# Performance work log

Measured on AMD Instinct MI355X. Metric: run time of the kernel, lower is better.

## Reference

```python
import jax, jax.numpy as jnp
import numpy as np

NC, M, D = 4, 512, 64
COMMITMENT_COST = 0.25


def setup_inputs() -> dict:
    key = jax.random.key(0)
    k1, k2 = jax.random.split(key)
    N = 65536
    x = jax.random.normal(k1, (N, NC * D), dtype=jnp.float32)
    # original init: uniform(-1/m, 1/m); randn*small keeps comparable scale
    embedding = jax.random.normal(k2, (NC, M, D), dtype=jnp.float32) * (1.0 / M)
    mask = jnp.ones((N, NC), dtype=jnp.float32)
    return {"x": x, "embedding": embedding, "mask": mask}


def reference(x, embedding, mask):
    nc, m, d = embedding.shape
    x_flat = x.reshape(-1, nc, d)                      # (N, nc, d)
    xd = jax.lax.stop_gradient(x_flat)                 # detached copy

    # squared-distance search expressed as a GEMM (same math as sum((x-e)^2)):
    x2 = jnp.sum(xd * xd, axis=-1)[:, :, None]
    e2 = jnp.sum(embedding * embedding, axis=-1)[None, :, :]
    xe = jnp.einsum('ncd,cmd->ncm', xd, embedding)
    distances = x2 - 2.0 * xe + e2

    indices = jnp.argmin(distances, axis=-1)           # (N, nc) int
    # gather nearest code vectors: (N, nc, d)
    quantized = embedding[jnp.arange(nc)[None, :], indices]
    quantized = quantized * mask[..., None]

    codebook_loss = jnp.mean((jax.lax.stop_gradient(x_flat) - quantized) ** 2)
    e_latent_loss = jnp.mean((x_flat - jax.lax.stop_gradient(quantized)) ** 2)
    commitment_loss = COMMITMENT_COST * e_latent_loss

    # straight-through estimator
    quantized_st = x_flat + jax.lax.stop_gradient(quantized - x_flat)
    quantized_st = quantized_st.reshape(x.shape)

    # perplexity via per-codebook histogram (avoids N x nc x m one-hot)
    counts = jax.vmap(lambda idx: jnp.bincount(idx, length=m))(indices.T)  # (nc, m)
    avg_probs = counts.astype(x.dtype) / x_flat.shape[0]
    perplexity = jnp.exp(-jnp.sum(avg_probs * jnp.log(avg_probs + 1e-10)))

    return (quantized_st, commitment_loss, codebook_loss, perplexity, indices)
```

## Files before the change

### kernel.cpp

```cpp
#include <hip/hip_runtime.h>
#include <math.h>
#include <float.h>

#define NTOK 65536
#define NCB  4
#define MCODE 512
#define DIM  64

#define QST_SIZE (NTOK * NCB * DIM)
#define IDX_OFF  (QST_SIZE + 3)

#define TOK_TILE  256
#define XS_STRIDE 68

#define WS_EH 0
#define WS_EL 262144
#define WS_D0 524288
#define WS_CNT 532480
#define WS_LOSS 540672

typedef _Float16 half8 __attribute__((ext_vector_type(8)));
typedef float floatx4 __attribute__((ext_vector_type(4)));

__global__ __launch_bounds__(256) void prep_kernel(const float* __restrict__ emb,
                                                   _Float16* __restrict__ eh,
                                                   _Float16* __restrict__ el,
                                                   float* __restrict__ d0,
                                                   int* __restrict__ counts,
                                                   float* __restrict__ lossSum) {
    int row = blockIdx.x * 256 + threadIdx.x;
    if (row >= NCB * MCODE) return;
    const float* src = emb + (size_t)row * DIM;
    _Float16* ph = eh + (size_t)row * DIM;
    _Float16* pl = el + (size_t)row * DIM;
    float s = 0.f;
#pragma unroll
    for (int j = 0; j < DIM / 8; ++j) {
        half8 h, l;
#pragma unroll
        for (int t = 0; t < 8; ++t) {
            float e = src[j * 8 + t];
            s += e * e;
            float f = e * 512.0f;
            _Float16 hi = (_Float16)f;
            float r = f - (float)hi;
            h[t] = hi;
            l[t] = (_Float16)r;
        }
        *(half8*)(ph + j * 8) = h;
        *(half8*)(pl + j * 8) = l;
    }
    d0[row] = 512.0f * s;
    counts[row] = 0;
    if (row == 0) *lossSum = 0.f;
}

__global__ __launch_bounds__(256) void vq_main(const float* __restrict__ x,
                                               const float* __restrict__ emb,
                                               const float* __restrict__ mask,
                                               const _Float16* __restrict__ eh,
                                               const _Float16* __restrict__ el,
                                               const float* __restrict__ d0,
                                               int* __restrict__ counts,
                                               float* __restrict__ lossSum,
                                               float* __restrict__ outQ,
                                               float* __restrict__ outIdx) {
    __shared__ float Xs[TOK_TILE * XS_STRIDE];
    __shared__ int   Is[TOK_TILE];
    __shared__ float wls[4];

    const int tid  = threadIdx.x;
    const int c    = blockIdx.y;
    const int n0tk = blockIdx.x * TOK_TILE;
    const int lane = tid & 63;
    const int w    = tid >> 6;
    const int col  = lane & 15;
    const int quad = lane >> 4;

#pragma unroll
    for (int i = 0; i < 16; ++i) {
        int q = tid + i * 256;
        int tok = q >> 4, d4 = q & 15;
        float4 v = *(const float4*)(x + (size_t)(n0tk + tok) * (NCB * DIM) + c * DIM + d4 * 4);
        *(float4*)(Xs + tok * XS_STRIDE + d4 * 4) = v;
    }
    __syncthreads();

    half8 Ahi[4][2], Alo[4][2];
#pragma unroll
    for (int s = 0; s < 4; ++s) {
        const float* xr = Xs + (w * 64 + s * 16 + col) * XS_STRIDE;
#pragma unroll
        for (int ks = 0; ks < 2; ++ks) {
            const float* p = xr + ks * 32 + quad * 8;
            half8 h, l;
#pragma unroll
            for (int t = 0; t < 8; ++t) {
                float f = p[t];
                _Float16 hi = (_Float16)f;
                float r = f - (float)hi;
                h[t] = hi;
                l[t] = (_Float16)r;
            }
            Ahi[s][ks] = h;
            Alo[s][ks] = l;
        }
    }

    float minv[4][4];
    int   mini[4][4];
#pragma unroll
    for (int s = 0; s < 4; ++s)
#pragma unroll
        for (int r = 0; r < 4; ++r) { minv[s][r] = FLT_MAX; mini[s][r] = 0; }

    const _Float16* ehc = eh + (size_t)c * MCODE * DIM;
    const _Float16* elc = el + (size_t)c * MCODE * DIM;
    const float*    d0c = d0 + c * MCODE;

#pragma unroll 2
    for (int nt = 0; nt < 32; ++nt) {
        const int nbase = nt * 16;
        const int n = nbase + col;
        const _Float16* bh = ehc + (size_t)n * DIM + quad * 8;
        const _Float16* bl = elc + (size_t)n * DIM + quad * 8;
        half8 Bh0 = *(const half8*)(bh);
        half8 Bh1 = *(const half8*)(bh + 32);
        half8 Bl0 = *(const half8*)(bl);
        half8 Bl1 = *(const half8*)(bl + 32);
        float d0v = d0c[n];

#pragma unroll
        for (int s = 0; s < 4; ++s) {
            floatx4 acc = {0.f, 0.f, 0.f, 0.f};
            acc = __builtin_amdgcn_mfma_f32_16x16x32_f16(Ahi[s][0], Bh0, acc, 0, 0, 0);
            acc = __builtin_amdgcn_mfma_f32_16x16x32_f16(Ahi[s][1], Bh1, acc, 0, 0, 0);
            acc = __builtin_amdgcn_mfma_f32_16x16x32_f16(Alo[s][0], Bh0, acc, 0, 0, 0);
            acc = __builtin_amdgcn_mfma_f32_16x16x32_f16(Alo[s][1], Bh1, acc, 0, 0, 0);
            acc = __builtin_amdgcn_mfma_f32_16x16x32_f16(Ahi[s][0], Bl0, acc, 0, 0, 0);
            acc = __builtin_amdgcn_mfma_f32_16x16x32_f16(Ahi[s][1], Bl1, acc, 0, 0, 0);
#pragma unroll
            for (int r = 0; r < 4; ++r) {
                float dv = fmaf(-2.f, acc[r], d0v);
                if (dv < minv[s][r]) { minv[s][r] = dv; mini[s][r] = n; }
            }
        }
    }

#pragma unroll
    for (int off = 1; off < 16; off <<= 1) {
#pragma unroll
        for (int s = 0; s < 4; ++s)
#pragma unroll
            for (int r = 0; r < 4; ++r) {
                float ov = __shfl_xor(minv[s][r], off);
                int   oi = __shfl_xor(mini[s][r], off);
                if (ov < minv[s][r] || (ov == minv[s][r] && oi < mini[s][r])) {
                    minv[s][r] = ov; mini[s][r] = oi;
                }
            }
    }
    if (col == 0) {
#pragma unroll
        for (int s = 0; s < 4; ++s)
#pragma unroll
            for (int r = 0; r < 4; ++r)
                Is[w * 64 + s * 16 + quad * 4 + r] = mini[s][r];
    }
    __syncthreads();

    {
        int idx = Is[tid];
        atomicAdd(&counts[c * MCODE + idx], 1);
        outIdx[(size_t)(n0tk + tid) * NCB + c] = (float)idx;
    }

    float lloss = 0.f;
#pragma unroll
    for (int i = 0; i < 16; ++i) {
        int q = tid + i * 256;
        int tok = q >> 4, d4 = q & 15;
        int idx = Is[tok];
        float mv = mask[(size_t)(n0tk + tok) * NCB + c];
        float4 e4 = *(const float4*)(emb + ((size_t)c * MCODE + idx) * DIM + d4 * 4);
        float4 x4 = *(const float4*)(Xs + tok * XS_STRIDE + d4 * 4);
        float qx = e4.x * mv, qy = e4.y * mv, qz = e4.z * mv, qw = e4.w * mv;
        float4 o;
        o.x = x4.x + (qx - x4.x);
        o.y = x4.y + (qy - x4.y);
        o.z = x4.z + (qz - x4.z);
        o.w = x4.w + (qw - x4.w);
        *(float4*)(outQ + (size_t)(n0tk + tok) * (NCB * DIM) + c * DIM + d4 * 4) = o;
        float dx = x4.x - qx, dy = x4.y - qy, dz = x4.z - qz, dw = x4.w - qw;
        lloss += dx * dx + dy * dy + dz * dz + dw * dw;
    }
#pragma unroll
    for (int off = 32; off > 0; off >>= 1) lloss += __shfl_xor(lloss, off);
    if ((tid & 63) == 0) wls[tid >> 6] = lloss;
    __syncthreads();
    if (tid == 0) {
        float s = wls[0] + wls[1] + wls[2] + wls[3];
        atomicAdd(lossSum, s);
    }
}

__global__ __launch_bounds__(256) void finalize_kernel(const int* __restrict__ counts,
                                                       const float* __restrict__ lossSum,
                                                       float* __restrict__ out) {
    __shared__ float wls[4];
    int tid = threadIdx.x;
    float s = 0.f;
#pragma unroll
    for (int i = 0; i < 8; ++i) {
        int j = tid + i * 256;
        float p = (float)counts[j] * (1.0f / 65536.0f);
        s += p * logf(p + 1e-10f);
    }
#pragma unroll
    for (int off = 32; off > 0; off >>= 1) s += __shfl_xor(s, off);
    if ((tid & 63) == 0) wls[tid >> 6] = s;
    __syncthreads();
    if (tid == 0) {
        float tot = wls[0] + wls[1] + wls[2] + wls[3];
        float L = *lossSum * (1.0f / (float)QST_SIZE);
        out[QST_SIZE + 0] = 0.25f * L;
        out[QST_SIZE + 1] = L;
        out[QST_SIZE + 2] = expf(-tot);
    }
}

extern "C" void kernel_launch(void* const* d_in, const int* in_sizes, int n_in,
                              void* d_out, int out_size, void* d_ws, size_t ws_size,
                              hipStream_t stream) {
    const float* x    = (const float*)d_in[0];
    const float* emb  = (const float*)d_in[1];
    const float* mask = (const float*)d_in[2];
    float* out = (float*)d_out;

    _Float16* eh   = (_Float16*)((char*)d_ws + WS_EH);
    _Float16* el   = (_Float16*)((char*)d_ws + WS_EL);
    float* d0      = (float*)((char*)d_ws + WS_D0);
    int*   counts  = (int*)((char*)d_ws + WS_CNT);
    float* lossSum = (float*)((char*)d_ws + WS_LOSS);

    prep_kernel<<<dim3(8), dim3(256), 0, stream>>>(emb, eh, el, d0, counts, lossSum);
    vq_main<<<dim3(NTOK / TOK_TILE, NCB), dim3(256), 0, stream>>>(
        x, emb, mask, eh, el, d0, counts, lossSum, out, out + IDX_OFF);
    finalize_kernel<<<dim3(1), dim3(256), 0, stream>>>(counts, lossSum, out);
}
```

Before: 222.3 us.

## Drop LDS staging of x and software-prefetch next codebook tile

Removes the 68KB shared-memory tile for x: the A fragments are now read straight from global memory with float4 loads, and x is re-read from global memory in the epilogue. This frees LDS, which should allow more blocks per CU, and removes one barrier. The codebook loop now double-buffers the B fragments and d0 in registers, loading tile nt+1 while the MFMAs run on tile nt. The cost is extra register pressure and a second global read of x, which will likely hit L2.

```diff
diff --git a/kernel.cpp b/kernel.cpp
--- a/kernel.cpp
+++ b/kernel.cpp
@@ -11,7 +11,6 @@
 #define IDX_OFF  (QST_SIZE + 3)
 
 #define TOK_TILE  256
-#define XS_STRIDE 68
 
 #define WS_EH 0
 #define WS_EL 262144
@@ -65,7 +64,6 @@
                                                float* __restrict__ lossSum,
                                                float* __restrict__ outQ,
                                                float* __restrict__ outIdx) {
-    __shared__ float Xs[TOK_TILE * XS_STRIDE];
     __shared__ int   Is[TOK_TILE];
     __shared__ float wls[4];
 
@@ -77,28 +75,21 @@
     const int col  = lane & 15;
     const int quad = lane >> 4;
 
-#pragma unroll
-    for (int i = 0; i < 16; ++i) {
-        int q = tid + i * 256;
-        int tok = q >> 4, d4 = q & 15;
-        float4 v = *(const float4*)(x + (size_t)(n0tk + tok) * (NCB * DIM) + c * DIM + d4 * 4);
-        *(float4*)(Xs + tok * XS_STRIDE + d4 * 4) = v;
-    }
-    __syncthreads();
-
     half8 Ahi[4][2], Alo[4][2];
 #pragma unroll
     for (int s = 0; s < 4; ++s) {
-        const float* xr = Xs + (w * 64 + s * 16 + col) * XS_STRIDE;
+        const float* xr = x + (size_t)(n0tk + w * 64 + s * 16 + col) * (NCB * DIM) + c * DIM;
 #pragma unroll
         for (int ks = 0; ks < 2; ++ks) {
             const float* p = xr + ks * 32 + quad * 8;
+            float4 f0 = *(const float4*)(p);
+            float4 f1 = *(const float4*)(p + 4);
+            float fv[8] = {f0.x, f0.y, f0.z, f0.w, f1.x, f1.y, f1.z, f1.w};
             half8 h, l;
 #pragma unroll
             for (int t = 0; t < 8; ++t) {
-                float f = p[t];
-                _Float16 hi = (_Float16)f;
-                float r = f - (float)hi;
+                _Float16 hi = (_Float16)fv[t];
+                float r = fv[t] - (float)hi;
                 h[t] = hi;
                 l[t] = (_Float16)r;
             }
@@ -114,22 +105,28 @@
 #pragma unroll
         for (int r = 0; r < 4; ++r) { minv[s][r] = FLT_MAX; mini[s][r] = 0; }
 
-    const _Float16* ehc = eh + (size_t)c * MCODE * DIM;
-    const _Float16* elc = el + (size_t)c * MCODE * DIM;
+    const _Float16* ehc = eh + (size_t)c * MCODE * DIM + (size_t)col * DIM + quad * 8;
+    const _Float16* elc = el + (size_t)c * MCODE * DIM + (size_t)col * DIM + quad * 8;
     const float*    d0c = d0 + c * MCODE;
 
-#pragma unroll 2
+    half8 Bh0 = *(const half8*)(ehc);
+    half8 Bh1 = *(const half8*)(ehc + 32);
+    half8 Bl0 = *(const half8*)(elc);
+    half8 Bl1 = *(const half8*)(elc + 32);
+    float d0v = d0c[col];
+
     for (int nt = 0; nt < 32; ++nt) {
-        const int nbase = nt * 16;
-        const int n = nbase + col;
-        const _Float16* bh = ehc + (size_t)n * DIM + quad * 8;
-        const _Float16* bl = elc + (size_t)n * DIM + quad * 8;
-        half8 Bh0 = *(const half8*)(bh);
-        half8 Bh1 = *(const half8*)(bh + 32);
-        half8 Bl0 = *(const half8*)(bl);
-        half8 Bl1 = *(const half8*)(bl + 32);
-        float d0v = d0c[n];
-
+        const int n = nt * 16 + col;
+        half8 Ch0, Ch1, Cl0, Cl1; float d0n;
+        if (nt < 31) {
+            const _Float16* bh = ehc + (size_t)(nt + 1) * 16 * DIM;
+            const _Float16* bl = elc + (size_t)(nt + 1) * 16 * DIM;
+            Ch0 = *(const half8*)(bh);
+            Ch1 = *(const half8*)(bh + 32);
+            Cl0 = *(const half8*)(bl);
+            Cl1 = *(const half8*)(bl + 32);
+            d0n = d0c[(nt + 1) * 16 + col];
+        }
 #pragma unroll
         for (int s = 0; s < 4; ++s) {
             floatx4 acc = {0.f, 0.f, 0.f, 0.f};
@@ -145,6 +142,9 @@
                 if (dv < minv[s][r]) { minv[s][r] = dv; mini[s][r] = n; }
             }
         }
+        if (nt < 31) {
+            Bh0 = Ch0; Bh1 = Ch1; Bl0 = Cl0; Bl1 = Cl1; d0v = d0n;
+        }
     }
 
 #pragma unroll
@@ -183,7 +183,7 @@
         int idx = Is[tok];
         float mv = mask[(size_t)(n0tk + tok) * NCB + c];
         float4 e4 = *(const float4*)(emb + ((size_t)c * MCODE + idx) * DIM + d4 * 4);
-        float4 x4 = *(const float4*)(Xs + tok * XS_STRIDE + d4 * 4);
+        float4 x4 = *(const float4*)(x + (size_t)(n0tk + tok) * (NCB * DIM) + c * DIM + d4 * 4);
         float qx = e4.x * mv, qy = e4.y * mv, qz = e4.z * mv, qw = e4.w * mv;
         float4 o;
         o.x = x4.x + (qx - x4.x);
```

Result: slower. 228.6 us (+2.8%).
